# Performance work log

Measured on AMD Instinct MI355X. Metric: run time of the kernel, lower is better.

The kernel has to match this reference:

```python
import jax, jax.numpy as jnp
import numpy as np

D_MODEL = 1024
N_HEADS = 16
D_HEAD = D_MODEL // N_HEADS


def setup_inputs() -> dict:
    key = jax.random.key(0)
    kx, kq, kk, kv, ko = jax.random.split(key, 5)
    s = 1.0 / np.sqrt(D_MODEL)
    return {
        "x": jax.random.normal(kx, (4, 2048, D_MODEL), dtype=jnp.float32),
        "Wq": jax.random.normal(kq, (D_MODEL, D_MODEL), dtype=jnp.float32) * s,
        "Wk": jax.random.normal(kk, (D_MODEL, D_MODEL), dtype=jnp.float32) * s,
        "Wv": jax.random.normal(kv, (D_MODEL, D_MODEL), dtype=jnp.float32) * s,
        "Wo": jax.random.normal(ko, (D_MODEL, D_MODEL), dtype=jnp.float32) * s,
    }


def reference(x, Wq, Wk, Wv, Wo):
    B, L, D = x.shape
    # Projections (torch Linear: y = x @ W.T)
    q = (x @ Wq.T).reshape(B, L, N_HEADS, D_HEAD).transpose(0, 2, 1, 3)  # [B,H,L,dh]
    k = (x @ Wk.T).reshape(B, L, N_HEADS, D_HEAD).transpose(0, 2, 1, 3)
    v = (x @ Wv.T).reshape(B, L, N_HEADS, D_HEAD).transpose(0, 2, 1, 3)
    scale = 1.0 / np.sqrt(D_HEAD).astype(np.float32)
    scores = jnp.einsum('bhqd,bhkd->bhqk', q, k) * scale  # [B,H,L,L]
    causal = jnp.tril(jnp.ones((L, L), dtype=bool))
    scores = jnp.where(causal[None, None], scores, -jnp.inf)
    attn = jax.nn.softmax(scores, axis=-1)
    out = jnp.einsum('bhqk,bhkd->bhqd', attn, v)  # [B,H,L,dh]
    out = out.transpose(0, 2, 1, 3).reshape(B, L, D)
    return out @ Wo.T
```

## Files before the change

kernel.cpp:

```cpp
#include <hip/hip_runtime.h>

typedef short bf16x8 __attribute__((ext_vector_type(8)));
typedef float f32x4 __attribute__((ext_vector_type(4)));
typedef unsigned short u16;

#define MFMA16x16x32(a, b, c) __builtin_amdgcn_mfma_f32_16x16x32_bf16((a), (b), (c), 0, 0, 0)

#define BATCH 4
#define SEQ 2048
#define DMODEL 1024
#define NHEADS 16
#define DHEAD 64
#define MROWS (BATCH * SEQ)

#define QSCALE 0.18033688011112443f

#if defined(__has_builtin)
#if __has_builtin(__builtin_amdgcn_exp2f)
#define EXP2(x) __builtin_amdgcn_exp2f(x)
#endif
#endif
#ifndef EXP2
#define EXP2(x) exp2f(x)
#endif

__device__ __forceinline__ u16 f2bf(float f) {
  unsigned u = __builtin_bit_cast(unsigned, f);
  u += 0x7fffu + ((u >> 16) & 1u);
  return (u16)(u >> 16);
}

__device__ __forceinline__ void gl_lds16(const u16* g, u16* l) {
  __builtin_amdgcn_global_load_lds((__attribute__((address_space(1))) void*)g,
                                   (__attribute__((address_space(3))) void*)l, 16, 0, 0);
}

__global__ void cvt_all(const float* __restrict__ x, const float* __restrict__ wq,
                        const float* __restrict__ wk, const float* __restrict__ wv,
                        const float* __restrict__ wo, u16* __restrict__ xb,
                        u16* __restrict__ wqb, u16* __restrict__ wkb, u16* __restrict__ wvb,
                        u16* __restrict__ wob) {
  int blk = blockIdx.x;
  const float* src;
  u16* dst;
  long off;
  if (blk < 8192) {
    src = x; dst = xb;
    off = (long)blk * 256 + threadIdx.x;
  } else {
    int ws = (blk - 8192) >> 10;
    int wb = (blk - 8192) & 1023;
    src = ws == 0 ? wq : ws == 1 ? wk : ws == 2 ? wv : wo;
    dst = ws == 0 ? wqb : ws == 1 ? wkb : ws == 2 ? wvb : wob;
    off = (long)wb * 256 + threadIdx.x;
  }
  float4 v = reinterpret_cast<const float4*>(src)[off];
  ushort4 o;
  o.x = f2bf(v.x); o.y = f2bf(v.y); o.z = f2bf(v.z); o.w = f2bf(v.w);
  reinterpret_cast<ushort4*>(dst)[off] = o;
}

__device__ __forceinline__ void gemm_core(const u16* __restrict__ A, const u16* __restrict__ Bm,
                                          int row0, int bcol0, u16* As, u16* Bs,
                                          f32x4 (*acc)[4], int tid) {
  const int lane = tid & 63, w = tid >> 6;
  const int wr = w >> 1, wc = w & 1;
  const int quad = lane >> 4, l16 = lane & 15;
  const int lr = lane >> 3;
  const int lcs = ((lane & 7) ^ lr) * 8;
  const int sw = (l16 & 7) * 8;

  const long abase = (long)(row0 + lr) * 1024 + lcs;
  const long bbase = (long)(bcol0 + lr) * 1024 + lcs;

  for (int k0 = 0; k0 < 1024; k0 += 64) {
#pragma unroll
    for (int i = 0; i < 4; i++) {
      int rb = i * 32 + w * 8;
      gl_lds16(&A[abase + (long)rb * 1024 + k0], &As[rb * 64]);
      gl_lds16(&Bm[bbase + (long)rb * 1024 + k0], &Bs[rb * 64]);
    }
    __syncthreads();
#pragma unroll
    for (int ks = 0; ks < 2; ks++) {
      bf16x8 af[4], bfr[4];
#pragma unroll
      for (int i = 0; i < 4; i++)
        af[i] = *reinterpret_cast<const bf16x8*>(
            &As[(wr * 64 + i * 16 + l16) * 64 + ((ks * 32 + quad * 8) ^ sw)]);
#pragma unroll
      for (int j = 0; j < 4; j++)
        bfr[j] = *reinterpret_cast<const bf16x8*>(
            &Bs[(wc * 64 + j * 16 + l16) * 64 + ((ks * 32 + quad * 8) ^ sw)]);
#pragma unroll
      for (int i = 0; i < 4; i++)
#pragma unroll
        for (int j = 0; j < 4; j++)
          acc[i][j] = MFMA16x16x32(af[i], bfr[j], acc[i][j]);
    }
    __syncthreads();
  }
}

__global__ __launch_bounds__(256) void gemm_qkv(const u16* __restrict__ xb,
                                                const u16* __restrict__ wqb,
                                                const u16* __restrict__ wkb,
                                                const u16* __restrict__ wvb,
                                                u16* __restrict__ qb, u16* __restrict__ kb,
                                                u16* __restrict__ vtb) {
  __shared__ u16 As[128 * 64];
  __shared__ u16 Bs[128 * 64];
  const int tid = threadIdx.x;
  const int lane = tid & 63, w = tid >> 6;
  const int wr = w >> 1, wc = w & 1;
  const int quad = lane >> 4, l16 = lane & 15;
  const int row0 = blockIdx.y * 128;
  const int col0 = blockIdx.x * 128;
  const int widx = col0 >> 10;
  const int bcol0 = col0 & 1023;
  const u16* Bm = widx == 0 ? wqb : (widx == 1 ? wkb : wvb);

  f32x4 acc[4][4] = {};
  gemm_core(xb, Bm, row0, bcol0, As, Bs, acc, tid);

#pragma unroll
  for (int i = 0; i < 4; i++)
#pragma unroll
    for (int j = 0; j < 4; j++)
#pragma unroll
      for (int r = 0; r < 4; r++) {
        int row = row0 + wr * 64 + i * 16 + quad * 4 + r;
        int col = bcol0 + wc * 64 + j * 16 + l16;
        float v = acc[i][j][r];
        int bh = ((row >> 11) << 4) | (col >> 6);
        if (widx == 0) {
          qb[(bh * SEQ + (row & 2047)) * DHEAD + (col & 63)] = f2bf(v * QSCALE);
        } else if (widx == 1) {
          kb[(bh * SEQ + (row & 2047)) * DHEAD + (col & 63)] = f2bf(v);
        } else {
          vtb[(bh * DHEAD + (col & 63)) * SEQ + (row & 2047)] = f2bf(v);
        }
      }
}

__global__ __launch_bounds__(256) void gemm_out(const u16* __restrict__ aob,
                                                const u16* __restrict__ wob,
                                                float* __restrict__ out) {
  __shared__ u16 As[128 * 64];
  __shared__ u16 Bs[128 * 64];
  const int tid = threadIdx.x;
  const int lane = tid & 63, w = tid >> 6;
  const int wr = w >> 1, wc = w & 1;
  const int quad = lane >> 4, l16 = lane & 15;
  const int row0 = blockIdx.y * 128;
  const int col0 = blockIdx.x * 128;

  f32x4 acc[4][4] = {};
  gemm_core(aob, wob, row0, col0, As, Bs, acc, tid);

#pragma unroll
  for (int i = 0; i < 4; i++)
#pragma unroll
    for (int j = 0; j < 4; j++)
#pragma unroll
      for (int r = 0; r < 4; r++) {
        int row = row0 + wr * 64 + i * 16 + quad * 4 + r;
        int col = col0 + wc * 64 + j * 16 + l16;
        out[(long)row * DMODEL + col] = acc[i][j][r];
      }
}

__global__ __launch_bounds__(256, 3) void attn_kernel(const u16* __restrict__ Q,
                                                      const u16* __restrict__ Kk,
                                                      const u16* __restrict__ Vt,
                                                      u16* __restrict__ Ao) {
  constexpr int PSTR = 72;
  __shared__ u16 Ksb[2][64 * 64];
  __shared__ u16 Vsb[2][64 * 64];
  __shared__ u16 Plds[4][32 * PSTR];
  const int tid = threadIdx.x;
  const int lane = tid & 63;
  const int w = tid >> 6;
  const int quad = lane >> 4, l16 = lane & 15;
  const int bh = blockIdx.x & 63;
  const int qt = 15 - (blockIdx.x >> 6);
  const int b = bh >> 4, h = bh & 15;
  const u16* Qh = Q + bh * SEQ * DHEAD;
  const u16* Kh = Kk + bh * SEQ * DHEAD;
  const u16* Vh = Vt + bh * DHEAD * SEQ;
  const int q0w = qt * 128 + w * 32;
  const int nkt = 2 * qt + 2;

  const int lr = lane >> 3;
  const int swcol = ((lane & 7) ^ lr) * 8;
  const int sw = (l16 & 7) * 8;

  bf16x8 onesf;
#pragma unroll
  for (int i = 0; i < 8; i++) onesf[i] = (short)0x3F80;

  bf16x8 qf[2][2];
#pragma unroll
  for (int rt = 0; rt < 2; rt++)
#pragma unroll
    for (int ks = 0; ks < 2; ks++)
      qf[rt][ks] = *reinterpret_cast<const bf16x8*>(
          &Qh[(q0w + rt * 16 + l16) * DHEAD + ks * 32 + quad * 8]);

  f32x4 o[2][4] = {};
  f32x4 lacc[2] = {};

  auto stage = [&](int kb, int bufi) {
    u16* Kd = Ksb[bufi];
    u16* Vd = Vsb[bufi];
#pragma unroll
    for (int i = 0; i < 2; i++) {
      int r = w * 16 + i * 8;
      gl_lds16(&Kh[(long)(kb + r + lr) * DHEAD + swcol], &Kd[r * 64]);
      gl_lds16(&Vh[(long)(r + lr) * SEQ + kb + swcol], &Vd[r * 64]);
    }
  };

  stage(0, 0);

  for (int kt = 0; kt < nkt; kt++) {
    const int kbase = kt * 64;
    asm volatile("s_waitcnt vmcnt(0) lgkmcnt(0)\n\ts_barrier" ::: "memory");
    if (kt + 1 < nkt) stage(kbase + 64, (kt + 1) & 1);

    const u16* Ks = Ksb[kt & 1];
    const u16* Vs = Vsb[kt & 1];

    if (kbase <= q0w + 31) {
      f32x4 s[2][4];
#pragma unroll
      for (int nt = 0; nt < 4; nt++) {
        bf16x8 kf0 = *reinterpret_cast<const bf16x8*>(
            &Ks[(nt * 16 + l16) * 64 + ((quad * 8) ^ sw)]);
        bf16x8 kf1 = *reinterpret_cast<const bf16x8*>(
            &Ks[(nt * 16 + l16) * 64 + ((32 + quad * 8) ^ sw)]);
#pragma unroll
        for (int rt = 0; rt < 2; rt++) {
          f32x4 z = {0.f, 0.f, 0.f, 0.f};
          z = MFMA16x16x32(qf[rt][0], kf0, z);
          s[rt][nt] = MFMA16x16x32(qf[rt][1], kf1, z);
        }
      }
      if (kbase + 63 > q0w) {
#pragma unroll
        for (int rt = 0; rt < 2; rt++)
#pragma unroll
          for (int nt = 0; nt < 4; nt++)
#pragma unroll
            for (int r = 0; r < 4; r++) {
              int qrow = q0w + rt * 16 + quad * 4 + r;
              int kcol = kbase + nt * 16 + l16;
              if (kcol > qrow) s[rt][nt][r] = -1e30f;
            }
      }
      u16* Pw = Plds[w];
#pragma unroll
      for (int rt = 0; rt < 2; rt++)
#pragma unroll
        for (int nt = 0; nt < 4; nt++)
#pragma unroll
          for (int r = 0; r < 4; r++) {
            float p = EXP2(s[rt][nt][r]);
            Pw[(rt * 16 + quad * 4 + r) * PSTR + nt * 16 + l16] =
                (u16)(__builtin_bit_cast(unsigned, p) >> 16);
          }
      asm volatile("s_waitcnt lgkmcnt(0)" ::: "memory");
      bf16x8 pa[2][2];
#pragma unroll
      for (int rt = 0; rt < 2; rt++)
#pragma unroll
        for (int hh = 0; hh < 2; hh++)
          pa[rt][hh] = *reinterpret_cast<const bf16x8*>(
              &Pw[(rt * 16 + l16) * PSTR + hh * 32 + quad * 8]);
#pragma unroll
      for (int nt2 = 0; nt2 < 4; nt2++) {
        bf16x8 vf0 = *reinterpret_cast<const bf16x8*>(
            &Vs[(nt2 * 16 + l16) * 64 + ((quad * 8) ^ sw)]);
        bf16x8 vf1 = *reinterpret_cast<const bf16x8*>(
            &Vs[(nt2 * 16 + l16) * 64 + ((32 + quad * 8) ^ sw)]);
#pragma unroll
        for (int rt = 0; rt < 2; rt++) {
          o[rt][nt2] = MFMA16x16x32(pa[rt][0], vf0, o[rt][nt2]);
          o[rt][nt2] = MFMA16x16x32(pa[rt][1], vf1, o[rt][nt2]);
        }
      }
#pragma unroll
      for (int rt = 0; rt < 2; rt++) {
        lacc[rt] = MFMA16x16x32(pa[rt][0], onesf, lacc[rt]);
        lacc[rt] = MFMA16x16x32(pa[rt][1], onesf, lacc[rt]);
      }
    }
  }

#pragma unroll
  for (int rt = 0; rt < 2; rt++) {
    float rl[4];
#pragma unroll
    for (int r = 0; r < 4; r++) rl[r] = 1.0f / lacc[rt][r];
#pragma unroll
    for (int nt2 = 0; nt2 < 4; nt2++)
#pragma unroll
      for (int r = 0; r < 4; r++) {
        int qrow = q0w + rt * 16 + quad * 4 + r;
        float v = o[rt][nt2][r] * rl[r];
        Ao[(b * SEQ + qrow) * DMODEL + h * DHEAD + nt2 * 16 + l16] = f2bf(v);
      }
  }
}

extern "C" void kernel_launch(void* const* d_in, const int* in_sizes, int n_in,
                              void* d_out, int out_size, void* d_ws, size_t ws_size,
                              hipStream_t stream) {
  const float* x = (const float*)d_in[0];
  const float* Wq = (const float*)d_in[1];
  const float* Wk = (const float*)d_in[2];
  const float* Wv = (const float*)d_in[3];
  const float* Wo = (const float*)d_in[4];
  float* out = (float*)d_out;

  u16* xb  = (u16*)d_ws;
  u16* wqb = xb  + MROWS * DMODEL;
  u16* wkb = wqb + DMODEL * DMODEL;
  u16* wvb = wkb + DMODEL * DMODEL;
  u16* wob = wvb + DMODEL * DMODEL;
  u16* qb  = wob + DMODEL * DMODEL;
  u16* kb  = qb  + MROWS * DMODEL;
  u16* vtb = kb  + MROWS * DMODEL;
  u16* aob = vtb + MROWS * DMODEL;

  cvt_all<<<12288, 256, 0, stream>>>(x, Wq, Wk, Wv, Wo, xb, wqb, wkb, wvb, wob);

  gemm_qkv<<<dim3(24, 64), 256, 0, stream>>>(xb, wqb, wkb, wvb, qb, kb, vtb);

  attn_kernel<<<BATCH * NHEADS * (SEQ / 128), 256, 0, stream>>>(qb, kb, vtb, aob);

  gemm_out<<<dim3(8, 64), 256, 0, stream>>>(aob, wob, out);
}
```

Before: 247.5 us.

## Double-buffer GEMM LDS tiles and swap grid axes for row-major block order

The projection GEMM core now uses two LDS buffers per operand. The next K-tile's global-to-LDS load is issued right after a single barrier, while MFMAs run on the current tile. This drops the second barrier per iteration and lets memory latency overlap with compute. The grid is also transposed so consecutive blocks walk along rows of the activation matrix, which changes L2 reuse of the weight tiles. The cost is double the LDS footprint (64 KB per block), which may lower occupancy.

```diff
diff --git a/kernel.cpp b/kernel.cpp
--- a/kernel.cpp
+++ b/kernel.cpp
@@ -61,8 +61,8 @@
 }
 
 __device__ __forceinline__ void gemm_core(const u16* __restrict__ A, const u16* __restrict__ Bm,
-                                          int row0, int bcol0, u16* As, u16* Bs,
-                                          f32x4 (*acc)[4], int tid) {
+                                          int row0, int bcol0, u16 (*As)[128 * 64],
+                                          u16 (*Bs)[128 * 64], f32x4 (*acc)[4], int tid) {
   const int lane = tid & 63, w = tid >> 6;
   const int wr = w >> 1, wc = w & 1;
   const int quad = lane >> 4, l16 = lane & 15;
@@ -73,32 +73,42 @@
   const long abase = (long)(row0 + lr) * 1024 + lcs;
   const long bbase = (long)(bcol0 + lr) * 1024 + lcs;
 
-  for (int k0 = 0; k0 < 1024; k0 += 64) {
+  auto stage = [&](int k0, int bufi) {
+    u16* Ad = As[bufi];
+    u16* Bd = Bs[bufi];
 #pragma unroll
     for (int i = 0; i < 4; i++) {
       int rb = i * 32 + w * 8;
-      gl_lds16(&A[abase + (long)rb * 1024 + k0], &As[rb * 64]);
-      gl_lds16(&Bm[bbase + (long)rb * 1024 + k0], &Bs[rb * 64]);
+      gl_lds16(&A[abase + (long)rb * 1024 + k0], &Ad[rb * 64]);
+      gl_lds16(&Bm[bbase + (long)rb * 1024 + k0], &Bd[rb * 64]);
     }
-    __syncthreads();
+  };
+
+  stage(0, 0);
+
+  for (int it = 0; it < 16; it++) {
+    asm volatile("s_waitcnt vmcnt(0) lgkmcnt(0)\n\ts_barrier" ::: "memory");
+    if (it + 1 < 16) stage((it + 1) * 64, (it + 1) & 1);
+
+    const u16* Asr = As[it & 1];
+    const u16* Bsr = Bs[it & 1];
 #pragma unroll
     for (int ks = 0; ks < 2; ks++) {
       bf16x8 af[4], bfr[4];
 #pragma unroll
       for (int i = 0; i < 4; i++)
         af[i] = *reinterpret_cast<const bf16x8*>(
-            &As[(wr * 64 + i * 16 + l16) * 64 + ((ks * 32 + quad * 8) ^ sw)]);
+            &Asr[(wr * 64 + i * 16 + l16) * 64 + ((ks * 32 + quad * 8) ^ sw)]);
 #pragma unroll
       for (int j = 0; j < 4; j++)
         bfr[j] = *reinterpret_cast<const bf16x8*>(
-            &Bs[(wc * 64 + j * 16 + l16) * 64 + ((ks * 32 + quad * 8) ^ sw)]);
+            &Bsr[(wc * 64 + j * 16 + l16) * 64 + ((ks * 32 + quad * 8) ^ sw)]);
 #pragma unroll
       for (int i = 0; i < 4; i++)
 #pragma unroll
         for (int j = 0; j < 4; j++)
           acc[i][j] = MFMA16x16x32(af[i], bfr[j], acc[i][j]);
     }
-    __syncthreads();
   }
 }
 
@@ -108,14 +118,14 @@
                                                 const u16* __restrict__ wvb,
                                                 u16* __restrict__ qb, u16* __restrict__ kb,
                                                 u16* __restrict__ vtb) {
-  __shared__ u16 As[128 * 64];
-  __shared__ u16 Bs[128 * 64];
+  __shared__ u16 As[2][128 * 64];
+  __shared__ u16 Bs[2][128 * 64];
   const int tid = threadIdx.x;
   const int lane = tid & 63, w = tid >> 6;
   const int wr = w >> 1, wc = w & 1;
   const int quad = lane >> 4, l16 = lane & 15;
-  const int row0 = blockIdx.y * 128;
-  const int col0 = blockIdx.x * 128;
+  const int row0 = blockIdx.x * 128;
+  const int col0 = blockIdx.y * 128;
   const int widx = col0 >> 10;
   const int bcol0 = col0 & 1023;
   const u16* Bm = widx == 0 ? wqb : (widx == 1 ? wkb : wvb);
@@ -146,14 +156,14 @@
 __global__ __launch_bounds__(256) void gemm_out(const u16* __restrict__ aob,
                                                 const u16* __restrict__ wob,
                                                 float* __restrict__ out) {
-  __shared__ u16 As[128 * 64];
-  __shared__ u16 Bs[128 * 64];
+  __shared__ u16 As[2][128 * 64];
+  __shared__ u16 Bs[2][128 * 64];
   const int tid = threadIdx.x;
   const int lane = tid & 63, w = tid >> 6;
   const int wr = w >> 1, wc = w & 1;
   const int quad = lane >> 4, l16 = lane & 15;
-  const int row0 = blockIdx.y * 128;
-  const int col0 = blockIdx.x * 128;
+  const int row0 = blockIdx.x * 128;
+  const int col0 = blockIdx.y * 128;
 
   f32x4 acc[4][4] = {};
   gemm_core(aob, wob, row0, col0, As, Bs, acc, tid);
@@ -335,9 +345,9 @@
 
   cvt_all<<<12288, 256, 0, stream>>>(x, Wq, Wk, Wv, Wo, xb, wqb, wkb, wvb, wob);
 
-  gemm_qkv<<<dim3(24, 64), 256, 0, stream>>>(xb, wqb, wkb, wvb, qb, kb, vtb);
+  gemm_qkv<<<dim3(64, 24), 256, 0, stream>>>(xb, wqb, wkb, wvb, qb, kb, vtb);
 
   attn_kernel<<<BATCH * NHEADS * (SEQ / 128), 256, 0, stream>>>(qb, kb, vtb, aob);
 
-  gemm_out<<<dim3(8, 64), 256, 0, stream>>>(aob, wob, out);
-}
+  gemm_out<<<dim3(64, 8), 256, 0, stream>>>(aob, wob, out);
+}
```

New measurement: 266.6 us. +7.7%, slower.
